# Kernel optimization log

Measured on AMD Instinct MI355X. Metric: run time of the kernel, lower is better.

The kernel has to match this reference:

```python
import jax, jax.numpy as jnp
import numpy as np

N = 50000      # nodes
E = 800000     # edges
D = 128        # in_dim == hidden_dim
L = 5          # num GIN layers
G = 1000       # graphs in batch


def setup_inputs() -> dict:
    key = jax.random.key(0)
    ks = jax.random.split(key, 6)
    s = 1.0 / np.sqrt(D)  # keep activations stable over 5 layers
    x = jax.random.normal(ks[0], (N, D), dtype=jnp.float32)
    edge_index = jax.random.randint(ks[1], (2, E), 0, N, dtype=jnp.int32)
    batch = jnp.sort(jax.random.randint(ks[2], (N,), 0, G, dtype=jnp.int32))
    W1s = jax.random.normal(ks[3], (L, D, D), dtype=jnp.float32) * s
    b1s = jnp.zeros((L, D), jnp.float32)
    W2s = jax.random.normal(ks[4], (L, D, D), dtype=jnp.float32) * s
    b2s = jnp.zeros((L, D), jnp.float32)
    Wh = jax.random.normal(ks[5], (D, 1), dtype=jnp.float32) * s
    bh = jnp.zeros((1,), jnp.float32)
    return {"x": x, "edge_index": edge_index, "batch": batch,
            "W1s": W1s, "b1s": b1s, "W2s": W2s, "b2s": b2s,
            "Wh": Wh, "bh": bh}


def reference(x, edge_index, batch, W1s, b1s, W2s, b2s, Wh, bh):
    src, dst = edge_index[0], edge_index[1]
    h = x
    for l in range(L):
        # GINConv with eps=0: mlp(x + sum_{j->i} x_j)
        aggr = jax.ops.segment_sum(h[src], dst, num_segments=N)  # [N, D]
        z = h + aggr
        z = jax.nn.relu(z @ W1s[l] + b1s[l]) @ W2s[l] + b2s[l]   # 2-layer MLP
        h = jax.nn.relu(z)  # outer F.relu; dropout is identity in eval
    # global mean pool per graph
    sums = jax.ops.segment_sum(h, batch, num_segments=G)                     # [G, D]
    cnts = jax.ops.segment_sum(jnp.ones((N, 1), h.dtype), batch, num_segments=G)
    pooled = sums / jnp.maximum(cnts, 1.0)
    return pooled @ Wh + bh  # [G, 1] logits
```

## Files before the change

kernel.cpp:

```cpp
#include <hip/hip_runtime.h>
#include <hip/hip_bf16.h>

#define D 128
#define SLOTS 64
#define CSTR 72
#define BCAP 9216

typedef short short8 __attribute__((ext_vector_type(8)));
typedef float f32x4 __attribute__((ext_vector_type(4)));
typedef unsigned short u16;
typedef unsigned int u32;

static __device__ __forceinline__ u16 f2bf(float f) {
  union { float f; unsigned u; } v; v.f = f;
  unsigned r = v.u + 0x7FFF + ((v.u >> 16) & 1);
  return (u16)(r >> 16);
}
static __device__ __forceinline__ float bf2f(u16 h) {
  union { unsigned u; float f; } v; v.u = ((unsigned)h) << 16;
  return v.f;
}

__global__ __launch_bounds__(1024) void prep_kernel(
    const int* __restrict__ src, const int* __restrict__ dst,
    const float* __restrict__ x, const float* __restrict__ W1,
    const float* __restrict__ W2, int* __restrict__ gcount,
    u32* __restrict__ bedge, u16* __restrict__ W1th, u16* __restrict__ W1tl,
    u16* __restrict__ W2th, u16* __restrict__ W2tl, u32* __restrict__ xp,
    u32* __restrict__ hp, int E, int nbk, int wtotal, int nPairs,
    int nA, int nB, int nC, int N, int rowsP) {
  __shared__ int cnt[128];
  __shared__ int base[128];
  int b = blockIdx.x, t = threadIdx.x;
  if (b < nA) {
    if (t < nbk) cnt[t] = 0;
    __syncthreads();
    int e = b * 1024 + t;
    int bk = 0, p = 0;
    u32 payload = 0;
    bool valid = e < E;
    if (valid) {
      int d = dst[e];
      bk = d >> 9;
      payload = ((u32)src[e] << 9) | (u32)(d & 511);
      p = atomicAdd(&cnt[bk], 1);
    }
    __syncthreads();
    if (t < nbk) base[t] = cnt[t] ? atomicAdd(&gcount[t], cnt[t]) : 0;
    __syncthreads();
    if (valid) {
      int pos = base[bk] + p;
      if (pos < BCAP) bedge[(size_t)bk * BCAP + pos] = payload;
    }
  } else if (b < nA + nB) {
    int idx = (b - nA) * 1024 + t;
    if (idx < wtotal) {
      int l = idx >> 14;
      int r = idx & 16383;
      int j = r & 7;
      int lane = (r >> 3) & 63;
      int tt = r >> 9;
      int kt = tt >> 3, nt = tt & 7;
      int k = kt * 32 + (lane >> 4) * 8 + j;
      int n = nt * 16 + (lane & 15);
      size_t s = (size_t)l * D * D + (size_t)k * D + n;
      float w1 = W1[s], w2 = W2[s];
      u16 h1 = f2bf(w1), h2 = f2bf(w2);
      W1th[idx] = h1; W1tl[idx] = f2bf(w1 - bf2f(h1));
      W2th[idx] = h2; W2tl[idx] = f2bf(w2 - bf2f(h2));
    }
  } else if (b < nA + nB + nC) {
    int i0 = (b - nA - nB) * 4096 + t * 4;
    if (i0 < nPairs) {
      int node = i0 >> 6, pr = i0 & 63;
      float4 f0 = ((const float4*)x)[i0 >> 1];
      float4 f1 = ((const float4*)x)[(i0 >> 1) + 1];
      uint4 o;
      o.x = ((u32)f2bf(f0.y) << 16) | f2bf(f0.x);
      o.y = ((u32)f2bf(f0.w) << 16) | f2bf(f0.z);
      o.z = ((u32)f2bf(f1.y) << 16) | f2bf(f1.x);
      o.w = ((u32)f2bf(f1.w) << 16) | f2bf(f1.z);
      *(uint4*)(xp + ((size_t)(pr >> 5) * rowsP + node) * 32 + (pr & 31)) = o;
    }
  } else {
    if (t < 64) {
      xp[((size_t)(t >> 5) * rowsP + N) * 32 + (t & 31)] = 0;
      hp[((size_t)(t >> 5) * rowsP + N) * 32 + (t & 31)] = 0;
    }
  }
}

__global__ __launch_bounds__(1024) void binB_kernel(
    const int* __restrict__ gcount, const u32* __restrict__ bedge,
    int* __restrict__ deg, u16* __restrict__ colidx, int N) {
  __shared__ int cnt2[512];
  int b = blockIdx.x;
  int t = threadIdx.x;
  if (t < 512) cnt2[t] = 0;
  __syncthreads();
  int count = min(gcount[b], BCAP);
  const u32* lst = bedge + (size_t)b * BCAP;
  for (int i = t; i < count; i += 1024) {
    u32 v = lst[i];
    int local = v & 511;
    int slot = atomicAdd(&cnt2[local], 1);
    if (slot < SLOTS)
      colidx[((size_t)(b << 9) + local) * CSTR + slot] = (u16)(v >> 9);
  }
  __syncthreads();
  if (t < 512) {
    int node = (b << 9) + t;
    if (node < N) deg[node] = min(cnt2[t], SLOTS);
  }
  for (int i = t; i < 512 * CSTR; i += 1024) {
    int local = i / CSTR;
    int slot = i - local * CSTR;
    int node = (b << 9) + local;
    if (node < N && slot >= min(cnt2[local], SLOTS))
      colidx[((size_t)(b << 9) + local) * CSTR + slot] = (u16)N;
  }
}

__global__ __launch_bounds__(256) void aggregate_kernel(
    const u32* __restrict__ hp, const int* __restrict__ deg,
    const u16* __restrict__ colidx, u32* __restrict__ zp, int N, int rowsP) {
  int p = blockIdx.x & 1;
  int chunk = blockIdx.x >> 1;
  int lane = threadIdx.x & 63;
  int wave = threadIdx.x >> 6;
  int g = lane >> 4, c = lane & 15;
  int node = chunk * 16 + wave * 4 + g;
  bool live = node < N;
  const uint2* hpp = (const uint2*)(hp + (size_t)p * rowsP * 32);
  int e = live ? deg[node] : 0;
  int em = max(e, __shfl_xor(e, 16, 64));
  em = max(em, __shfl_xor(em, 32, 64));
  const u16* nbr = colidx + (size_t)(live ? node : 0) * CSTR;
  uint2 s = hpp[(size_t)(live ? node : N) * 16 + c];
  float a0 = bf2f((u16)(s.x & 0xffff)), a1 = bf2f((u16)(s.x >> 16));
  float a2 = bf2f((u16)(s.y & 0xffff)), a3 = bf2f((u16)(s.y >> 16));
  for (int k = 0; k < em; k += 8) {
    int idx[8];
    uint2 v[8];
#pragma unroll
    for (int i = 0; i < 8; ++i) idx[i] = nbr[k + i];
#pragma unroll
    for (int i = 0; i < 8; ++i) v[i] = hpp[(size_t)idx[i] * 16 + c];
#pragma unroll
    for (int i = 0; i < 8; ++i) {
      a0 += bf2f((u16)(v[i].x & 0xffff)); a1 += bf2f((u16)(v[i].x >> 16));
      a2 += bf2f((u16)(v[i].y & 0xffff)); a3 += bf2f((u16)(v[i].y >> 16));
    }
  }
  if (live) {
    uint2 o;
    o.x = ((u32)f2bf(a1) << 16) | f2bf(a0);
    o.y = ((u32)f2bf(a3) << 16) | f2bf(a2);
    ((uint2*)(zp + (size_t)p * rowsP * 32))[(size_t)node * 16 + c] = o;
  }
}

template <int STAGE>
__global__ __launch_bounds__(256) void gemm_kernel(
    const u16* __restrict__ A, const u16* __restrict__ Wth, const u16* __restrict__ Wtl,
    const float* __restrict__ bias, u16* __restrict__ outp,
    const float* __restrict__ Wh, const int* __restrict__ batch, float* __restrict__ gsum,
    int nrows, int rowsP) {
  __shared__ __attribute__((aligned(16))) u16 ldsW[32768];
  u16* ldsWh = ldsW;
  u16* ldsWl = ldsW + 16384;
  int tid = threadIdx.x;
  {
    const uint4* gh = (const uint4*)Wth;
    const uint4* gl = (const uint4*)Wtl;
    uint4 th[8], tl[8];
#pragma unroll
    for (int i = 0; i < 8; ++i) { th[i] = gh[tid + i * 256]; tl[i] = gl[tid + i * 256]; }
    uint4* lh = (uint4*)ldsWh;
    uint4* ll = (uint4*)ldsWl;
#pragma unroll
    for (int i = 0; i < 8; ++i) { lh[tid + i * 256] = th[i]; ll[tid + i * 256] = tl[i]; }
  }
  int wave = tid >> 6, lane = tid & 63;
  int quad = lane >> 4, l16 = lane & 15;
  int rowbase = blockIdx.x * 128 + wave * 32;
  int mc0 = min(rowbase + l16, nrows - 1);
  int mc1 = min(rowbase + 16 + l16, nrows - 1);

  short8 a0[4], a1[4];
#pragma unroll
  for (int kt = 0; kt < 4; ++kt) {
    if (STAGE == 0) {
      const u16* base = A + ((size_t)(kt >> 1) * rowsP) * 64 + (kt & 1) * 32 + quad * 8;
      a0[kt] = *(const short8*)(base + (size_t)mc0 * 64);
      a1[kt] = *(const short8*)(base + (size_t)mc1 * 64);
    } else {
      a0[kt] = *(const short8*)(A + (size_t)mc0 * D + kt * 32 + quad * 8);
      a1[kt] = *(const short8*)(A + (size_t)mc1 * D + kt * 32 + quad * 8);
    }
  }

  __syncthreads();

  f32x4 acc[2][8];
  f32x4 zero = {0.f, 0.f, 0.f, 0.f};
#pragma unroll
  for (int mt = 0; mt < 2; ++mt)
#pragma unroll
    for (int nt = 0; nt < 8; ++nt) acc[mt][nt] = zero;

#pragma unroll
  for (int kt = 0; kt < 4; ++kt) {
#pragma unroll
    for (int nt = 0; nt < 8; ++nt) {
      int fo = ((kt * 8 + nt) * 64 + lane) * 8;
      short8 bh = *(const short8*)(ldsWh + fo);
      short8 bl = *(const short8*)(ldsWl + fo);
      acc[0][nt] = __builtin_amdgcn_mfma_f32_16x16x32_bf16(a0[kt], bh, acc[0][nt], 0, 0, 0);
      acc[0][nt] = __builtin_amdgcn_mfma_f32_16x16x32_bf16(a0[kt], bl, acc[0][nt], 0, 0, 0);
      acc[1][nt] = __builtin_amdgcn_mfma_f32_16x16x32_bf16(a1[kt], bh, acc[1][nt], 0, 0, 0);
      acc[1][nt] = __builtin_amdgcn_mfma_f32_16x16x32_bf16(a1[kt], bl, acc[1][nt], 0, 0, 0);
    }
  }

  if (STAGE == 2) {
    float dotr[2][4] = {{0.f, 0.f, 0.f, 0.f}, {0.f, 0.f, 0.f, 0.f}};
#pragma unroll
    for (int nt = 0; nt < 8; ++nt) {
      int col = nt * 16 + l16;
      float bv = bias[col];
      float wv = Wh[col];
#pragma unroll
      for (int mt = 0; mt < 2; ++mt)
#pragma unroll
        for (int r = 0; r < 4; ++r)
          dotr[mt][r] += fmaxf(acc[mt][nt][r] + bv, 0.f) * wv;
    }
#pragma unroll
    for (int m = 1; m < 16; m <<= 1) {
#pragma unroll
      for (int mt = 0; mt < 2; ++mt)
#pragma unroll
        for (int r = 0; r < 4; ++r) dotr[mt][r] += __shfl_xor(dotr[mt][r], m, 64);
    }
    if (l16 == 0) {
#pragma unroll
      for (int mt = 0; mt < 2; ++mt)
#pragma unroll
        for (int r = 0; r < 4; ++r) {
          int row = rowbase + mt * 16 + quad * 4 + r;
          if (row < nrows) atomicAdd(&gsum[batch[row]], dotr[mt][r]);
        }
    }
  } else {
    __syncthreads();
#pragma unroll
    for (int nt = 0; nt < 8; ++nt) {
      float bv = bias[nt * 16 + l16];
#pragma unroll
      for (int mt = 0; mt < 2; ++mt)
#pragma unroll
        for (int r = 0; r < 4; ++r) {
          int lrow = wave * 32 + mt * 16 + quad * 4 + r;
          ldsW[lrow * 136 + nt * 16 + l16] = f2bf(fmaxf(acc[mt][nt][r] + bv, 0.f));
        }
    }
    __syncthreads();
#pragma unroll
    for (int i = 0; i < 8; ++i) {
      int chunk = i * 256 + tid;
      int r = chunk >> 4;
      int cc = (chunk & 15) * 8;
      int row = blockIdx.x * 128 + r;
      if (row < nrows) {
        uint4 v = *(const uint4*)(ldsW + r * 136 + cc);
        if (STAGE == 0) {
          *(uint4*)(outp + (size_t)row * D + cc) = v;
        } else {
          *(uint4*)(outp + ((size_t)(cc >> 6) * rowsP + row) * 64 + (cc & 63)) = v;
        }
      }
    }
  }
}

__global__ void pool_final_kernel(const float* __restrict__ gsum, const int* __restrict__ batch,
                                  const float* __restrict__ bh, float* __restrict__ out,
                                  int G, int N) {
  int g = blockIdx.x * 256 + threadIdx.x;
  if (g >= G) return;
  int lo = 0, hi = N;
  while (lo < hi) { int mid = (lo + hi) >> 1; if (batch[mid] < g) lo = mid + 1; else hi = mid; }
  int lo2 = lo, hi2 = N;
  while (lo2 < hi2) { int mid = (lo2 + hi2) >> 1; if (batch[mid] < g + 1) lo2 = mid + 1; else hi2 = mid; }
  int c = lo2 - lo;
  out[g] = gsum[g] / fmaxf((float)c, 1.f) + bh[0];
}

extern "C" void kernel_launch(void* const* d_in, const int* in_sizes, int n_in,
                              void* d_out, int out_size, void* d_ws, size_t ws_size,
                              hipStream_t stream) {
  const float* x   = (const float*)d_in[0];
  const int* eidx  = (const int*)d_in[1];
  const int* batch = (const int*)d_in[2];
  const float* W1s = (const float*)d_in[3];
  const float* b1s = (const float*)d_in[4];
  const float* W2s = (const float*)d_in[5];
  const float* b2s = (const float*)d_in[6];
  const float* Wh  = (const float*)d_in[7];
  const float* bh  = (const float*)d_in[8];
  float* out = (float*)d_out;

  int N = in_sizes[0] / D;
  int E = in_sizes[1] / 2;
  int G = out_size;
  int L = in_sizes[3] / (D * D);
  int nbk = (N + 511) >> 9;
  int wtotal = L * D * D;
  int nPairs = N * D / 2;
  int rowsP = N + 1;

  const int* src = eidx;
  const int* dst = eidx + E;

  char* p = (char*)d_ws;
  auto alloc = [&](size_t b) { char* r = p; p += (b + 255) & ~(size_t)255; return r; };
  u16*   hpnl   = (u16*)  alloc((size_t)2 * rowsP * 64 * 2);
  u16*   xpnl   = (u16*)  alloc((size_t)2 * rowsP * 64 * 2);
  u16*   zpnl   = (u16*)  alloc((size_t)2 * rowsP * 64 * 2);
  u16*   yb     = (u16*)  alloc((size_t)N * D * 2);
  size_t zbytes = (size_t)G * 4 + 512;
  char*  zblk   =         alloc(zbytes);
  float* gsum   = (float*)zblk;
  int*   gcount = (int*)(zblk + (size_t)G * 4);
  int*   deg    = (int*)  alloc((size_t)N * 4);
  u16*   colidx = (u16*)  alloc((size_t)N * CSTR * 2);
  u32*   bedge  = (u32*)  alloc((size_t)128 * BCAP * 4);
  u16*   W1th   = (u16*)  alloc((size_t)L * D * D * 2);
  u16*   W1tl   = (u16*)  alloc((size_t)L * D * D * 2);
  u16*   W2th   = (u16*)  alloc((size_t)L * D * D * 2);
  u16*   W2tl   = (u16*)  alloc((size_t)L * D * D * 2);

  hipMemsetAsync(zblk, 0, zbytes, stream);

  int nA = (E + 1023) / 1024;
  int nB = (wtotal + 1023) / 1024;
  int nC = (nPairs / 4 + 1023) / 1024;
  prep_kernel<<<nA + nB + nC + 1, 1024, 0, stream>>>(
      src, dst, x, W1s, W2s, gcount, bedge, W1th, W1tl, W2th, W2tl,
      (u32*)xpnl, (u32*)hpnl, E, nbk, wtotal, nPairs, nA, nB, nC, N, rowsP);
  binB_kernel<<<nbk, 1024, 0, stream>>>(gcount, bedge, deg, colidx, N);

  int agg_blocks = 2 * ((N + 15) / 16);
  int gemm_blocks = (N + 127) / 128;
  for (int l = 0; l < L; ++l) {
    const u16* hin = (l == 0) ? xpnl : hpnl;
    size_t wo = (size_t)l * D * D;
    aggregate_kernel<<<agg_blocks, 256, 0, stream>>>(
        (const u32*)hin, deg, colidx, (u32*)zpnl, N, rowsP);
    gemm_kernel<0><<<gemm_blocks, 256, 0, stream>>>(
        zpnl, W1th + wo, W1tl + wo, b1s + (size_t)l * D, yb,
        nullptr, nullptr, nullptr, N, rowsP);
    if (l < L - 1) {
      gemm_kernel<1><<<gemm_blocks, 256, 0, stream>>>(
          yb, W2th + wo, W2tl + wo, b2s + (size_t)l * D, hpnl,
          nullptr, nullptr, nullptr, N, rowsP);
    } else {
      gemm_kernel<2><<<gemm_blocks, 256, 0, stream>>>(
          yb, W2th + wo, W2tl + wo, b2s + (size_t)l * D, nullptr,
          Wh, batch, gsum, N, rowsP);
    }
  }
  pool_final_kernel<<<(G + 255) / 256, 256, 0, stream>>>(gsum, batch, bh, out, G, N);
}
```

Before: 398.7 us.

## Split GEMM output columns across two blocks to halve LDS and double grid

Each GEMM block now computes only 64 of the 128 output columns, selected by the low bit of the block index, so the grid doubles. Weight staging in LDS is halved to 32KB and the output staging stride shrinks to 72, which should allow more resident blocks per CU and more parallelism across the 391-row-tile grid. The cost is that each A row tile is loaded twice, once by each column-half block. In the final stage, partial head dot-products are atomically accumulated from both halves.

```diff
diff --git a/kernel.cpp b/kernel.cpp
--- a/kernel.cpp
+++ b/kernel.cpp
@@ -166,24 +166,35 @@
     const float* __restrict__ bias, u16* __restrict__ outp,
     const float* __restrict__ Wh, const int* __restrict__ batch, float* __restrict__ gsum,
     int nrows, int rowsP) {
-  __shared__ __attribute__((aligned(16))) u16 ldsW[32768];
+  __shared__ __attribute__((aligned(16))) u16 ldsW[16384];
   u16* ldsWh = ldsW;
-  u16* ldsWl = ldsW + 16384;
+  u16* ldsWl = ldsW + 8192;
   int tid = threadIdx.x;
+  int nb = blockIdx.x & 1;
+  int rb = blockIdx.x >> 1;
   {
     const uint4* gh = (const uint4*)Wth;
     const uint4* gl = (const uint4*)Wtl;
-    uint4 th[8], tl[8];
-#pragma unroll
-    for (int i = 0; i < 8; ++i) { th[i] = gh[tid + i * 256]; tl[i] = gl[tid + i * 256]; }
-    uint4* lh = (uint4*)ldsWh;
-    uint4* ll = (uint4*)ldsWl;
-#pragma unroll
-    for (int i = 0; i < 8; ++i) { lh[tid + i * 256] = th[i]; ll[tid + i * 256] = tl[i]; }
+    uint4 th[4], tl[4];
+#pragma unroll
+    for (int i = 0; i < 4; ++i) {
+      int idx = i * 256 + tid;
+      int lf = idx >> 6;
+      int u4 = idx & 63;
+      int gf = (lf >> 2) * 8 + nb * 4 + (lf & 3);
+      th[i] = gh[gf * 64 + u4];
+      tl[i] = gl[gf * 64 + u4];
+    }
+    uint4* lh = (uint4*)ldsW;
+#pragma unroll
+    for (int i = 0; i < 4; ++i) {
+      lh[i * 256 + tid] = th[i];
+      lh[1024 + i * 256 + tid] = tl[i];
+    }
   }
   int wave = tid >> 6, lane = tid & 63;
   int quad = lane >> 4, l16 = lane & 15;
-  int rowbase = blockIdx.x * 128 + wave * 32;
+  int rowbase = rb * 128 + wave * 32;
   int mc0 = min(rowbase + l16, nrows - 1);
   int mc1 = min(rowbase + 16 + l16, nrows - 1);
 
@@ -202,39 +213,39 @@
 
   __syncthreads();
 
-  f32x4 acc[2][8];
+  f32x4 acc[2][4];
   f32x4 zero = {0.f, 0.f, 0.f, 0.f};
 #pragma unroll
   for (int mt = 0; mt < 2; ++mt)
 #pragma unroll
-    for (int nt = 0; nt < 8; ++nt) acc[mt][nt] = zero;
+    for (int nt = 0; nt < 4; ++nt) acc[mt][nt] = zero;
 
 #pragma unroll
   for (int kt = 0; kt < 4; ++kt) {
 #pragma unroll
-    for (int nt = 0; nt < 8; ++nt) {
-      int fo = ((kt * 8 + nt) * 64 + lane) * 8;
+    for (int ntl = 0; ntl < 4; ++ntl) {
+      int fo = ((kt * 4 + ntl) * 64 + lane) * 8;
       short8 bh = *(const short8*)(ldsWh + fo);
       short8 bl = *(const short8*)(ldsWl + fo);
-      acc[0][nt] = __builtin_amdgcn_mfma_f32_16x16x32_bf16(a0[kt], bh, acc[0][nt], 0, 0, 0);
-      acc[0][nt] = __builtin_amdgcn_mfma_f32_16x16x32_bf16(a0[kt], bl, acc[0][nt], 0, 0, 0);
-      acc[1][nt] = __builtin_amdgcn_mfma_f32_16x16x32_bf16(a1[kt], bh, acc[1][nt], 0, 0, 0);
-      acc[1][nt] = __builtin_amdgcn_mfma_f32_16x16x32_bf16(a1[kt], bl, acc[1][nt], 0, 0, 0);
+      acc[0][ntl] = __builtin_amdgcn_mfma_f32_16x16x32_bf16(a0[kt], bh, acc[0][ntl], 0, 0, 0);
+      acc[0][ntl] = __builtin_amdgcn_mfma_f32_16x16x32_bf16(a0[kt], bl, acc[0][ntl], 0, 0, 0);
+      acc[1][ntl] = __builtin_amdgcn_mfma_f32_16x16x32_bf16(a1[kt], bh, acc[1][ntl], 0, 0, 0);
+      acc[1][ntl] = __builtin_amdgcn_mfma_f32_16x16x32_bf16(a1[kt], bl, acc[1][ntl], 0, 0, 0);
     }
   }
 
   if (STAGE == 2) {
     float dotr[2][4] = {{0.f, 0.f, 0.f, 0.f}, {0.f, 0.f, 0.f, 0.f}};
 #pragma unroll
-    for (int nt = 0; nt < 8; ++nt) {
-      int col = nt * 16 + l16;
+    for (int ntl = 0; ntl < 4; ++ntl) {
+      int col = nb * 64 + ntl * 16 + l16;
       float bv = bias[col];
       float wv = Wh[col];
 #pragma unroll
       for (int mt = 0; mt < 2; ++mt)
 #pragma unroll
         for (int r = 0; r < 4; ++r)
-          dotr[mt][r] += fmaxf(acc[mt][nt][r] + bv, 0.f) * wv;
+          dotr[mt][r] += fmaxf(acc[mt][ntl][r] + bv, 0.f) * wv;
     }
 #pragma unroll
     for (int m = 1; m < 16; m <<= 1) {
@@ -255,29 +266,29 @@
   } else {
     __syncthreads();
 #pragma unroll
-    for (int nt = 0; nt < 8; ++nt) {
-      float bv = bias[nt * 16 + l16];
+    for (int ntl = 0; ntl < 4; ++ntl) {
+      float bv = bias[nb * 64 + ntl * 16 + l16];
 #pragma unroll
       for (int mt = 0; mt < 2; ++mt)
 #pragma unroll
         for (int r = 0; r < 4; ++r) {
           int lrow = wave * 32 + mt * 16 + quad * 4 + r;
-          ldsW[lrow * 136 + nt * 16 + l16] = f2bf(fmaxf(acc[mt][nt][r] + bv, 0.f));
+          ldsW[lrow * 72 + ntl * 16 + l16] = f2bf(fmaxf(acc[mt][ntl][r] + bv, 0.f));
         }
     }
     __syncthreads();
 #pragma unroll
-    for (int i = 0; i < 8; ++i) {
+    for (int i = 0; i < 4; ++i) {
       int chunk = i * 256 + tid;
-      int r = chunk >> 4;
-      int cc = (chunk & 15) * 8;
-      int row = blockIdx.x * 128 + r;
+      int r = chunk >> 3;
+      int cc = (chunk & 7) * 8;
+      int row = rb * 128 + r;
       if (row < nrows) {
-        uint4 v = *(const uint4*)(ldsW + r * 136 + cc);
+        uint4 v = *(const uint4*)(ldsW + r * 72 + cc);
         if (STAGE == 0) {
-          *(uint4*)(outp + (size_t)row * D + cc) = v;
+          *(uint4*)(outp + (size_t)row * D + nb * 64 + cc) = v;
         } else {
-          *(uint4*)(outp + ((size_t)(cc >> 6) * rowsP + row) * 64 + (cc & 63)) = v;
+          *(uint4*)(outp + ((size_t)nb * rowsP + row) * 64 + cc) = v;
         }
       }
     }
@@ -352,7 +363,7 @@
   binB_kernel<<<nbk, 1024, 0, stream>>>(gcount, bedge, deg, colidx, N);
 
   int agg_blocks = 2 * ((N + 15) / 16);
-  int gemm_blocks = (N + 127) / 128;
+  int gemm_blocks = 2 * ((N + 127) / 128);
   for (int l = 0; l < L; ++l) {
     const u16* hin = (l == 0) ? xpnl : hpnl;
     size_t wo = (size_t)l * D * D;
```

Result: slower. 406.9 us (+2.1%).
